# Kernel optimization log

Hardware: AMD Instinct MI355X
Metric: run time of the kernel (lower is better)

## Reference

```python
import jax, jax.numpy as jnp
import numpy as np

B, S, T = 8, 2048, 128  # batch, seq_len, token_embedding_dim (== dep_transformed_dim, required by source bug)


def setup_inputs() -> dict:
    key = jax.random.key(0)
    k1, k2, k3, k4, k5, k6, k7 = jax.random.split(key, 7)
    sT = 1.0 / np.sqrt(T)
    sS = 1.0 / np.sqrt(S)
    return {
        "token_embeddings": jax.random.normal(k1, (B, S, T), jnp.float32),
        "dep_embeddings": jax.random.normal(k2, (B, S, T), jnp.float32),  # dead input (source bug), kept for fidelity
        "dep_heads": jax.random.randint(k3, (B, S), 0, S, jnp.int32),
        # composition_transform = Bilinear(T, T, T): weight [T_out, T_in1, T_in2], bias [T_out]
        "W_comp": jax.random.uniform(k4, (T, T, T), jnp.float32, -sT, sT),
        "b_comp": jax.random.uniform(k5, (T,), jnp.float32, -sT, sT),
        # reduction_transform = Linear(S, 1)
        "w_red": jax.random.uniform(k6, (1, S), jnp.float32, -sS, sS),
        "b_red": jax.random.uniform(k7, (1,), jnp.float32, -sS, sS),
    }


def reference(token_embeddings, dep_embeddings, dep_heads, W_comp, b_comp, w_red, b_red):
    # Faithful to source semantics (including the bug where dep_transform output is
    # discarded and tanh is applied to token_embeddings instead):
    #   dense[b,i,j,:] = tanh( bilinear(token[b,j], mask(i==heads[b,j]) * tanh(token[b,j])) )
    #   out[b,i,t]     = sum_j w_red[j] * dense[b,i,j,t] + b_red
    # Where mask is zero, bilinear collapses to its bias, so we never materialize
    # the [B,S,S,T] tensor: compute the 'active' value per token j and scatter-add
    # the delta vs. the bias-only baseline into row i = dep_heads[b,j].
    h = jnp.tanh(token_embeddings)                                   # [B,S,T]
    val = jnp.einsum('bsp,tpq,bsq->bst', token_embeddings, W_comp, h) + b_comp  # [B,S,T]
    act = jnp.tanh(val)                                              # active (masked-in) values
    base_val = jnp.tanh(b_comp)                                      # [T] value where mask is zero
    w = w_red[0]                                                     # [S], reduction weights over j
    base = jnp.sum(w) * base_val + b_red[0]                          # [T] bias-only row
    delta = w[None, :, None] * (act - base_val)                      # [B,S,T]
    b_idx = jnp.arange(token_embeddings.shape[0])[:, None]           # [B,1]
    out = base + jnp.zeros_like(act).at[b_idx, dep_heads].add(delta) # scatter over head rows
    return out
```

## Files before the change

kernel.cpp:

```cpp
#include <hip/hip_runtime.h>
#include <hip/hip_fp16.h>
#include <math.h>

#define S_LEN 2048
#define T_DIM 128
#define BM 128
#define TN 64
#define NBLK 256
#define TOKR 132

typedef _Float16 half8 __attribute__((ext_vector_type(8)));
typedef _Float16 half4t __attribute__((ext_vector_type(4)));
typedef float floatx16 __attribute__((ext_vector_type(16)));

__device__ __forceinline__ float tanh_fast(float x) {
  return 1.0f - __fdividef(2.0f, 1.0f + __expf(2.0f * x));
}

__global__ __launch_bounds__(256) void prep_kernel(
    const float* __restrict__ W, const float* __restrict__ w_red,
    const float* __restrict__ b_comp, const float* __restrict__ b_red,
    _Float16* __restrict__ W16f, float* __restrict__ out) {
  const int blk = blockIdx.x;
  const int tid = threadIdx.x;
  if (blk < 1024) {
    const int t = blk >> 3;
    const int qh = (blk >> 2) & 1;
    const int it = blk & 3;
    const int tc = t >> 5, tl = t & 31;
    const int e8 = it * 256 + tid;
    const int p = e8 >> 3;
    const int q = qh * 64 + (e8 & 7) * 8;
    const float* src = W + (size_t)t * 16384 + (size_t)p * 128 + q;
    const float4 v0 = *(const float4*)src;
    const float4 v1 = *(const float4*)(src + 4);
    half8 h;
    h[0] = (_Float16)v0.x; h[1] = (_Float16)v0.y;
    h[2] = (_Float16)v0.z; h[3] = (_Float16)v0.w;
    h[4] = (_Float16)v1.x; h[5] = (_Float16)v1.y;
    h[6] = (_Float16)v1.z; h[7] = (_Float16)v1.w;
    const int kc = q >> 4, lh2 = (q >> 3) & 1;
    *(half8*)(W16f + ((size_t)((p * 4 + tc) * 8 + kc)) * 512 + lh2 * 256 + tl * 8) = h;
  } else {
    __shared__ float red4[4];
    float part = 0.f;
#pragma unroll
    for (int i = 0; i < 8; ++i) part += w_red[tid * 8 + i];
#pragma unroll
    for (int off = 32; off > 0; off >>= 1) part += __shfl_down(part, off, 64);
    if ((tid & 63) == 0) red4[tid >> 6] = part;
    __syncthreads();
    const float Sw = red4[0] + red4[1] + red4[2] + red4[3];
    const float br = b_red[0];
    const size_t base = (size_t)(blk - 1024) * 1024 + (size_t)tid * 4;
    const int t0 = (int)(base & 127);
    float4 v;
    v.x = Sw * tanh_fast(b_comp[t0 + 0]) + br;
    v.y = Sw * tanh_fast(b_comp[t0 + 1]) + br;
    v.z = Sw * tanh_fast(b_comp[t0 + 2]) + br;
    v.w = Sw * tanh_fast(b_comp[t0 + 3]) + br;
    *(float4*)(out + base) = v;
  }
}

__global__ __launch_bounds__(512, 2) void main_kernel(
    const float* __restrict__ tok, const int* __restrict__ heads,
    const _Float16* __restrict__ W16f, const float* __restrict__ b_comp,
    const float* __restrict__ w_red, float* __restrict__ out) {
  __shared__ _Float16 tokT2[128 * TOKR];
  __shared__ float red[2][BM * TN];

  const int tid = threadIdx.x;
  const int lane = tid & 63;
  const int kh = tid >> 6;
  const int l31 = lane & 31;
  const int lh = lane >> 5;
  const int blk = blockIdx.x;
  const int th = blk & 1;
  const int mb = blk >> 1;
  const int pstag = ((blk >> 3) * 4) & 127;
  const size_t tokbase = (size_t)mb * BM * T_DIM;

#pragma unroll
  for (int it = 0; it < 8; ++it) {
    const int f = it * 512 + tid;
    const int m = f >> 5;
    const int p0 = (f & 31) * 4;
    const float4 v = *(const float4*)(tok + tokbase + (size_t)m * 128 + p0);
    const int mi = (m & 31) * 4 + (m >> 5);
    const float vv[4] = {v.x, v.y, v.z, v.w};
#pragma unroll
    for (int jj = 0; jj < 4; ++jj) {
      const int p = p0 + jj;
      const int col = mi ^ (((p + (p >> 3)) & 7) << 2);
      tokT2[p * TOKR + col] = (_Float16)vv[jj];
    }
  }

  half8 h16[4];
#pragma unroll
  for (int mh = 0; mh < 4; ++mh) {
    const int m = mh * 32 + l31;
    const int q0 = kh * 16 + lh * 8;
    const float4 v0 = *(const float4*)(tok + tokbase + (size_t)m * 128 + q0);
    const float4 v1 = *(const float4*)(tok + tokbase + (size_t)m * 128 + q0 + 4);
    h16[mh][0] = (_Float16)tanh_fast(v0.x);
    h16[mh][1] = (_Float16)tanh_fast(v0.y);
    h16[mh][2] = (_Float16)tanh_fast(v0.z);
    h16[mh][3] = (_Float16)tanh_fast(v0.w);
    h16[mh][4] = (_Float16)tanh_fast(v1.x);
    h16[mh][5] = (_Float16)tanh_fast(v1.y);
    h16[mh][6] = (_Float16)tanh_fast(v1.z);
    h16[mh][7] = (_Float16)tanh_fast(v1.w);
  }

  int off[2];
#pragma unroll
  for (int tt = 0; tt < 2; ++tt)
    off[tt] = (((th * 2 + tt) * 8 + kh) << 9) + lane * 8;

  half8 bf0[2], bf1[2], bf2[2];
  half4t tk0, tk1, tk2;

  auto loadB = [&](half8 (&bf)[2], int p) {
    const int pp = (p + pstag) & 127;
    const _Float16* wp = W16f + (size_t)pp * 16384;
    bf[0] = *(const half8*)(wp + off[0]);
    bf[1] = *(const half8*)(wp + off[1]);
  };
  auto loadT = [&](half4t& tk, int p) {
    const int pp = (p + pstag) & 127;
    const int col = (l31 * 4) ^ (((pp + (pp >> 3)) & 7) << 2);
    tk = *(const half4t*)(tokT2 + pp * TOKR + col);
  };

  loadB(bf0, 0);
  loadB(bf1, 1);

  floatx16 acc[4][2];
#pragma unroll
  for (int mh = 0; mh < 4; ++mh)
#pragma unroll
    for (int tt = 0; tt < 2; ++tt)
#pragma unroll
      for (int r = 0; r < 16; ++r) acc[mh][tt][r] = 0.f;

  __syncthreads();

  auto compute = [&](half8 (&bf)[2], half4t tk) {
#pragma unroll
    for (int mh = 0; mh < 4; ++mh) {
      half8 a = h16[mh] * tk[mh];
      acc[mh][0] = __builtin_amdgcn_mfma_f32_32x32x16_f16(a, bf[0], acc[mh][0], 0, 0, 0);
      acc[mh][1] = __builtin_amdgcn_mfma_f32_32x32x16_f16(a, bf[1], acc[mh][1], 0, 0, 0);
    }
  };

  loadT(tk0, 0);
  loadT(tk1, 1);
  for (int p = 0; p < 126; p += 3) {
    loadB(bf2, p + 2);  loadT(tk2, p + 2);
    compute(bf0, tk0);
    loadB(bf0, p + 3);  loadT(tk0, p + 3);
    compute(bf1, tk1);
    loadB(bf1, p + 4);  loadT(tk1, p + 4);
    compute(bf2, tk2);
  }
  compute(bf0, tk0);
  compute(bf1, tk1);

  __syncthreads();
  {
    float* R = &red[kh & 1][0];
    const int g = kh >> 1;
#pragma unroll
    for (int phase = 0; phase < 4; ++phase) {
      if (g == phase) {
#pragma unroll
        for (int mh = 0; mh < 4; ++mh)
#pragma unroll
          for (int tt = 0; tt < 2; ++tt) {
            const int t_loc = tt * 32 + l31;
#pragma unroll
            for (int r = 0; r < 16; ++r) {
              const int m_loc = mh * 32 + (r & 3) + 8 * (r >> 2) + 4 * lh;
              const int addr = m_loc * TN + t_loc;
              if (phase == 0) R[addr] = acc[mh][tt][r];
              else            R[addr] += acc[mh][tt][r];
            }
          }
      }
      __syncthreads();
    }
  }

  const int t_loc = tid & 63;
  const int mgrp = tid >> 6;
  const int t = th * 64 + t_loc;
  const float bc = b_comp[t];
  const float tb = tanh_fast(bc);
#pragma unroll 4
  for (int mi = 0; mi < 16; ++mi) {
    const int m_loc = mi * 8 + mgrp;
    const int gm = mb * BM + m_loc;
    const int head = heads[gm];
    const float wr = w_red[gm & 2047];
    const float v = red[0][m_loc * TN + t_loc] + red[1][m_loc * TN + t_loc] + bc;
    atomicAdd(out + ((size_t)(gm >> 11) * S_LEN + head) * T_DIM + t,
              wr * (tanh_fast(v) - tb));
  }
}

extern "C" void kernel_launch(void* const* d_in, const int* in_sizes, int n_in,
                              void* d_out, int out_size, void* d_ws, size_t ws_size,
                              hipStream_t stream) {
  const float* tok    = (const float*)d_in[0];
  const int*   heads  = (const int*)d_in[2];
  const float* W      = (const float*)d_in[3];
  const float* b_comp = (const float*)d_in[4];
  const float* w_red  = (const float*)d_in[5];
  const float* b_red  = (const float*)d_in[6];
  float* out = (float*)d_out;

  _Float16* W16f = (_Float16*)d_ws;

  prep_kernel<<<3072, 256, 0, stream>>>(W, w_red, b_comp, b_red, W16f, out);
  main_kernel<<<NBLK, 512, 0, stream>>>(tok, heads, W16f, b_comp, w_red, out);
}
```

Baseline: 151.6 us.

## Coarsen prep kernel work per thread and prefetch weight fragments before token staging

The prep kernel now has each thread convert 16 contiguous weight values, writing two fragments, and each output-init block fills 8 float4 chunks. Together these cut the prep grid from 3072 to 768 blocks. In the main kernel, the first two weight-fragment global loads are issued before the token transpose into shared memory, so their latency overlaps that staging work. Shared memory is merged into one manually carved buffer. The trade-offs are fewer prep blocks to hide latency, prep weight reads that are strided across threads, and possibly higher register pressure from the early loads.

Result: faster. 148.1 us (-2.3%).

```diff
diff --git a/kernel.cpp b/kernel.cpp
--- a/kernel.cpp
+++ b/kernel.cpp
@@ -8,6 +8,7 @@
 #define TN 64
 #define NBLK 256
 #define TOKR 132
+#define TOK_BYTES 33792
 
 typedef _Float16 half8 __attribute__((ext_vector_type(8)));
 typedef _Float16 half4t __attribute__((ext_vector_type(4)));
@@ -23,43 +24,49 @@
     _Float16* __restrict__ W16f, float* __restrict__ out) {
   const int blk = blockIdx.x;
   const int tid = threadIdx.x;
-  if (blk < 1024) {
-    const int t = blk >> 3;
-    const int qh = (blk >> 2) & 1;
-    const int it = blk & 3;
-    const int tc = t >> 5, tl = t & 31;
-    const int e8 = it * 256 + tid;
-    const int p = e8 >> 3;
-    const int q = qh * 64 + (e8 & 7) * 8;
-    const float* src = W + (size_t)t * 16384 + (size_t)p * 128 + q;
-    const float4 v0 = *(const float4*)src;
-    const float4 v1 = *(const float4*)(src + 4);
-    half8 h;
-    h[0] = (_Float16)v0.x; h[1] = (_Float16)v0.y;
-    h[2] = (_Float16)v0.z; h[3] = (_Float16)v0.w;
-    h[4] = (_Float16)v1.x; h[5] = (_Float16)v1.y;
-    h[6] = (_Float16)v1.z; h[7] = (_Float16)v1.w;
-    const int kc = q >> 4, lh2 = (q >> 3) & 1;
-    *(half8*)(W16f + ((size_t)((p * 4 + tc) * 8 + kc)) * 512 + lh2 * 256 + tl * 8) = h;
+  if (blk < 512) {
+    const int p = blk & 127;
+    const int tc = blk >> 7;
+    const int kc = tid >> 5;
+    const int tl = tid & 31;
+    const int t = tc * 32 + tl;
+    const float* src = W + (size_t)t * 16384 + (size_t)p * 128 + kc * 16;
+    const float4 a = *(const float4*)(src);
+    const float4 b = *(const float4*)(src + 4);
+    const float4 c = *(const float4*)(src + 8);
+    const float4 d = *(const float4*)(src + 12);
+    half8 lo, hi;
+    lo[0] = (_Float16)a.x; lo[1] = (_Float16)a.y;
+    lo[2] = (_Float16)a.z; lo[3] = (_Float16)a.w;
+    lo[4] = (_Float16)b.x; lo[5] = (_Float16)b.y;
+    lo[6] = (_Float16)b.z; lo[7] = (_Float16)b.w;
+    hi[0] = (_Float16)c.x; hi[1] = (_Float16)c.y;
+    hi[2] = (_Float16)c.z; hi[3] = (_Float16)c.w;
+    hi[4] = (_Float16)d.x; hi[5] = (_Float16)d.y;
+    hi[6] = (_Float16)d.z; hi[7] = (_Float16)d.w;
+    _Float16* fb = W16f + ((size_t)((p * 4 + tc) * 8 + kc)) * 512;
+    *(half8*)(fb + tl * 8) = lo;
+    *(half8*)(fb + 256 + tl * 8) = hi;
   } else {
     __shared__ float red4[4];
     float part = 0.f;
 #pragma unroll
-    for (int i = 0; i < 8; ++i) part += w_red[tid * 8 + i];
+    for (int i = 0; i < 8; ++i) part += w_red[i * 256 + tid];
 #pragma unroll
     for (int off = 32; off > 0; off >>= 1) part += __shfl_down(part, off, 64);
     if ((tid & 63) == 0) red4[tid >> 6] = part;
     __syncthreads();
     const float Sw = red4[0] + red4[1] + red4[2] + red4[3];
     const float br = b_red[0];
-    const size_t base = (size_t)(blk - 1024) * 1024 + (size_t)tid * 4;
-    const int t0 = (int)(base & 127);
+    const int t0 = (tid * 4) & 127;
     float4 v;
     v.x = Sw * tanh_fast(b_comp[t0 + 0]) + br;
     v.y = Sw * tanh_fast(b_comp[t0 + 1]) + br;
     v.z = Sw * tanh_fast(b_comp[t0 + 2]) + br;
     v.w = Sw * tanh_fast(b_comp[t0 + 3]) + br;
-    *(float4*)(out + base) = v;
+    float* dst = out + (size_t)(blk - 512) * 8192 + (size_t)tid * 4;
+#pragma unroll
+    for (int k = 0; k < 8; ++k) *(float4*)(dst + k * 1024) = v;
   }
 }
 
@@ -67,8 +74,10 @@
     const float* __restrict__ tok, const int* __restrict__ heads,
     const _Float16* __restrict__ W16f, const float* __restrict__ b_comp,
     const float* __restrict__ w_red, float* __restrict__ out) {
-  __shared__ _Float16 tokT2[128 * TOKR];
-  __shared__ float red[2][BM * TN];
+  __shared__ __align__(16) char smembuf[99328];
+  _Float16* const tokT2 = (_Float16*)smembuf;
+  float* const red0 = (float*)(smembuf + TOK_BYTES);
+  float* const red1 = (float*)(smembuf + TOK_BYTES + 32768);
 
   const int tid = threadIdx.x;
   const int lane = tid & 63;
@@ -81,6 +90,30 @@
   const int pstag = ((blk >> 3) * 4) & 127;
   const size_t tokbase = (size_t)mb * BM * T_DIM;
 
+  int off[2];
+#pragma unroll
+  for (int tt = 0; tt < 2; ++tt)
+    off[tt] = (((th * 2 + tt) * 8 + kh) << 9) + lane * 8;
+
+  half8 bf0[2], bf1[2], bf2[2];
+  half4t tk0, tk1, tk2;
+  half8 h16[4];
+
+  auto loadB = [&](half8 (&bf)[2], int p) {
+    const int pp = (p + pstag) & 127;
+    const _Float16* wp = W16f + (size_t)pp * 16384;
+    bf[0] = *(const half8*)(wp + off[0]);
+    bf[1] = *(const half8*)(wp + off[1]);
+  };
+  auto loadT = [&](half4t& tk, int p) {
+    const int pp = (p + pstag) & 127;
+    const int col = (l31 * 4) ^ (((pp + (pp >> 3)) & 7) << 2);
+    tk = *(const half4t*)(tokT2 + pp * TOKR + col);
+  };
+
+  loadB(bf0, 0);
+  loadB(bf1, 1);
+
 #pragma unroll
   for (int it = 0; it < 8; ++it) {
     const int f = it * 512 + tid;
@@ -97,7 +130,6 @@
     }
   }
 
-  half8 h16[4];
 #pragma unroll
   for (int mh = 0; mh < 4; ++mh) {
     const int m = mh * 32 + l31;
@@ -114,29 +146,6 @@
     h16[mh][7] = (_Float16)tanh_fast(v1.w);
   }
 
-  int off[2];
-#pragma unroll
-  for (int tt = 0; tt < 2; ++tt)
-    off[tt] = (((th * 2 + tt) * 8 + kh) << 9) + lane * 8;
-
-  half8 bf0[2], bf1[2], bf2[2];
-  half4t tk0, tk1, tk2;
-
-  auto loadB = [&](half8 (&bf)[2], int p) {
-    const int pp = (p + pstag) & 127;
-    const _Float16* wp = W16f + (size_t)pp * 16384;
-    bf[0] = *(const half8*)(wp + off[0]);
-    bf[1] = *(const half8*)(wp + off[1]);
-  };
-  auto loadT = [&](half4t& tk, int p) {
-    const int pp = (p + pstag) & 127;
-    const int col = (l31 * 4) ^ (((pp + (pp >> 3)) & 7) << 2);
-    tk = *(const half4t*)(tokT2 + pp * TOKR + col);
-  };
-
-  loadB(bf0, 0);
-  loadB(bf1, 1);
-
   floatx16 acc[4][2];
 #pragma unroll
   for (int mh = 0; mh < 4; ++mh)
@@ -171,7 +180,7 @@
 
   __syncthreads();
   {
-    float* R = &red[kh & 1][0];
+    float* R = (kh & 1) ? red1 : red0;
     const int g = kh >> 1;
 #pragma unroll
     for (int phase = 0; phase < 4; ++phase) {
@@ -205,7 +214,7 @@
     const int gm = mb * BM + m_loc;
     const int head = heads[gm];
     const float wr = w_red[gm & 2047];
-    const float v = red[0][m_loc * TN + t_loc] + red[1][m_loc * TN + t_loc] + bc;
+    const float v = red0[m_loc * TN + t_loc] + red1[m_loc * TN + t_loc] + bc;
     atomicAdd(out + ((size_t)(gm >> 11) * S_LEN + head) * T_DIM + t,
               wr * (tanh_fast(v) - tb));
   }
@@ -224,6 +233,6 @@
 
   _Float16* W16f = (_Float16*)d_ws;
 
-  prep_kernel<<<3072, 256, 0, stream>>>(W, w_red, b_comp, b_red, W16f, out);
+  prep_kernel<<<768, 256, 0, stream>>>(W, w_red, b_comp, b_red, W16f, out);
   main_kernel<<<NBLK, 512, 0, stream>>>(tok, heads, W16f, b_comp, w_red, out);
 }
```
